# Performance work log

Hardware: AMD Instinct MI355X
Metric: run time of the kernel (lower is better)

Reference implementation:

```python
import jax, jax.numpy as jnp
import numpy as np

N_INST = 131072      # total patches across all bags
D_EMB = 512          # VGG16 pooling='max' output dim
ATT_UNITS = 128
CLS_UNITS = 512
NUM_BAGS = 256


def setup_inputs() -> dict:
    key = jax.random.key(0)
    ks = jax.random.split(key, 16)
    first_emb = jax.random.normal(ks[0], (N_INST, D_EMB), dtype=jnp.float32)
    first_lab = jnp.sort(jax.random.randint(ks[1], (N_INST,), 0, NUM_BAGS)).astype(jnp.int64)
    s = 0.02
    return {
        "first_emb": first_emb,
        "first_lab": first_lab,
        # first-level attention head: Dense(tanh) -> Dense(1, sigmoid)
        "W_a1": jax.random.normal(ks[2], (D_EMB, ATT_UNITS), dtype=jnp.float32) * s,
        "b_a1": jnp.zeros((ATT_UNITS,), dtype=jnp.float32),
        "w_o1": jax.random.normal(ks[3], (ATT_UNITS, 1), dtype=jnp.float32) * s,
        "b_o1": jnp.zeros((1,), dtype=jnp.float32),
        # second-level attention head
        "W_a2": jax.random.normal(ks[4], (D_EMB, ATT_UNITS), dtype=jnp.float32) * s,
        "b_a2": jnp.zeros((ATT_UNITS,), dtype=jnp.float32),
        "w_o2": jax.random.normal(ks[5], (ATT_UNITS, 1), dtype=jnp.float32) * s,
        "b_o2": jnp.zeros((1,), dtype=jnp.float32),
        # classifier: Dense(CLS_UNITS, linear) -> Dense(1, sigmoid)
        "W_c": jax.random.normal(ks[6], (D_EMB, CLS_UNITS), dtype=jnp.float32) * s,
        "b_c": jnp.zeros((CLS_UNITS,), dtype=jnp.float32),
        "w_out": jax.random.normal(ks[7], (CLS_UNITS, 1), dtype=jnp.float32) * s,
        "b_out": jnp.zeros((1,), dtype=jnp.float32),
    }


def reference(first_emb, first_lab, W_a1, b_a1, w_o1, b_o1,
              W_a2, b_a2, w_o2, b_o2, W_c, b_c, w_out, b_out):
    # --- first-level (instance) attention ---
    a1 = jnp.tanh(first_emb @ W_a1 + b_a1)                 # [N, A]
    att1 = jax.nn.sigmoid(a1 @ w_o1 + b_o1)                # [N, 1]
    # tf: transpose(softmax(transpose(att))) == softmax over the N axis (global)
    fst_att = jax.nn.softmax(att1, axis=0)                 # [N, 1]
    # --- per-bag attention-weighted sum (fused segment reduce) ---
    # replaces the python loop of gather_nd + matmul over contiguous bags
    second_emb = jax.ops.segment_sum(fst_att * first_emb, first_lab,
                                     num_segments=NUM_BAGS)  # [B, D]
    # --- second-level (bag) attention ---
    a2 = jnp.tanh(second_emb @ W_a2 + b_a2)                # [B, A]
    att2 = jax.nn.sigmoid(a2 @ w_o2 + b_o2)                # [B, 1]
    snd_att = jax.nn.softmax(att2.T, axis=-1)              # [1, B]
    outer_bag_emb = snd_att @ second_emb                   # [1, D]
    # --- classifier (dropout is identity at inference) ---
    h = outer_bag_emb @ W_c + b_c                          # [1, CLS]
    pred = jax.nn.sigmoid(h @ w_out + b_out)               # [1, 1]
    return pred
```

## Files before the change

kernel.cpp:

```cpp
#include <hip/hip_runtime.h>
#include <cstdint>
#include <cstddef>

#define N_INST 131072
#define D_EMB  512
#define ATT    128
#define NBAGS  256
#define TILE_I 32
#define LDA    520

typedef __attribute__((ext_vector_type(8))) short  bf16x8;
typedef __attribute__((ext_vector_type(4))) float  f32x4;
typedef __attribute__((ext_vector_type(4))) unsigned short u16x4;


__device__ inline unsigned short f2b(float f) {
    unsigned u = __builtin_bit_cast(unsigned, f);
    u += 0x7FFFu + ((u >> 16) & 1u);
    return (unsigned short)(u >> 16);
}

__device__ inline float fast_tanh(float x) {
    float e = __expf(2.f * x);
    return 1.f - 2.f / (e + 1.f);
}

__global__ __launch_bounds__(256) void k_prep_wt(
    const float* __restrict__ Wa1, unsigned short* __restrict__ Wt)
{
    const int n = blockIdx.x;
    for (int k = threadIdx.x; k < D_EMB; k += 256)
        Wt[(size_t)n * D_EMB + k] = f2b(Wa1[(size_t)k * ATT + n]);
}

__global__ __launch_bounds__(256, 4) void k_att1(
    const float* __restrict__ emb, const int* __restrict__ lab,
    const unsigned short* __restrict__ Wt, const float* __restrict__ ba1,
    const float* __restrict__ wo1, const float* __restrict__ bo1,
    float* __restrict__ rawr, int R, float* __restrict__ Z1)
{
    __shared__ unsigned short Ash[TILE_I * LDA];
    __shared__ float att4[4][TILE_I];
    __shared__ float sval[TILE_I];
    __shared__ int   labs[TILE_I];

    const int t  = threadIdx.x;
    const int w  = t >> 6;
    const int l  = t & 63;
    const int l4 = l & 15;
    const int h4 = l >> 4;
    const size_t i0 = (size_t)blockIdx.x * TILE_I;
    float* __restrict__ raw = rawr + (size_t)(blockIdx.x % R) * (NBAGS * D_EMB);

    if (t < TILE_I) labs[t] = lab[i0 + t];

    float ba1v[2], wo1v[2];
    #pragma unroll
    for (int nt = 0; nt < 2; ++nt) {
        int c = 16 * (2 * w + nt) + l4;
        ba1v[nt] = ba1[c];
        wo1v[nt] = wo1[c];
    }

    bf16x8 bfrag[2][16];
    #pragma unroll
    for (int nt = 0; nt < 2; ++nt) {
        const int n = 16 * (2 * w + nt) + l4;
        #pragma unroll
        for (int ks = 0; ks < 16; ++ks)
            bfrag[nt][ks] = *reinterpret_cast<const bf16x8*>(
                &Wt[(size_t)n * D_EMB + 32 * ks + 8 * h4]);
    }

    #pragma unroll
    for (int g = 0; g < 2; ++g) {
        float4 v[8];
        #pragma unroll
        for (int j = 0; j < 8; ++j) {
            int idx = (g * 8 + j) * 256 + t;
            int row = idx >> 7;
            int c4  = (idx & 127) * 4;
            v[j] = *reinterpret_cast<const float4*>(&emb[(i0 + row) * D_EMB + c4]);
        }
        #pragma unroll
        for (int j = 0; j < 8; ++j) {
            int idx = (g * 8 + j) * 256 + t;
            int row = idx >> 7;
            int c4  = (idx & 127) * 4;
            u16x4 b = { f2b(v[j].x), f2b(v[j].y), f2b(v[j].z), f2b(v[j].w) };
            *reinterpret_cast<u16x4*>(&Ash[row * LDA + c4]) = b;
        }
    }
    __syncthreads();

    f32x4 acc[2][2];
    #pragma unroll
    for (int rt = 0; rt < 2; ++rt) {
        acc[rt][0] = (f32x4){0.f, 0.f, 0.f, 0.f};
        acc[rt][1] = (f32x4){0.f, 0.f, 0.f, 0.f};
    }
    #pragma unroll
    for (int rt = 0; rt < 2; ++rt) {
        #pragma unroll
        for (int ks = 0; ks < 16; ++ks) {
            bf16x8 af = *reinterpret_cast<const bf16x8*>(
                &Ash[(16 * rt + l4) * LDA + 32 * ks + 8 * h4]);
            acc[rt][0] = __builtin_amdgcn_mfma_f32_16x16x32_bf16(
                af, bfrag[0][ks], acc[rt][0], 0, 0, 0);
            acc[rt][1] = __builtin_amdgcn_mfma_f32_16x16x32_bf16(
                af, bfrag[1][ks], acc[rt][1], 0, 0, 0);
        }
    }

    #pragma unroll
    for (int rt = 0; rt < 2; ++rt) {
        #pragma unroll
        for (int reg = 0; reg < 4; ++reg) {
            float p = fast_tanh(acc[rt][0][reg] + ba1v[0]) * wo1v[0]
                    + fast_tanh(acc[rt][1][reg] + ba1v[1]) * wo1v[1];
            p += __shfl_xor(p, 1);
            p += __shfl_xor(p, 2);
            p += __shfl_xor(p, 4);
            p += __shfl_xor(p, 8);
            if (l4 == 0) att4[w][16 * rt + 4 * h4 + reg] = p;
        }
    }
    __syncthreads();
    if (t < TILE_I) {
        float a  = att4[0][t] + att4[1][t] + att4[2][t] + att4[3][t] + bo1[0];
        float sg = 1.f / (1.f + __expf(-a));
        sval[t]  = __expf(sg);
    }
    __syncthreads();
    if (t < TILE_I) {
        float z = sval[t];
        z += __shfl_xor(z, 1);
        z += __shfl_xor(z, 2);
        z += __shfl_xor(z, 4);
        z += __shfl_xor(z, 8);
        z += __shfl_xor(z, 16);
        if (t == 0) atomicAdd(Z1, z);
    }

    int s0 = 0;
    while (s0 < TILE_I) {
        int bag = labs[s0];
        int s1 = s0 + 1;
        while (s1 < TILE_I && labs[s1] == bag) ++s1;
        float a0 = 0.f, a1 = 0.f;
        #pragma unroll 8
        for (int ii = s0; ii < s1; ++ii) {
            unsigned u = *reinterpret_cast<const unsigned*>(
                &Ash[(size_t)ii * LDA + 2 * t]);
            float lo = __builtin_bit_cast(float, u << 16);
            float hi = __builtin_bit_cast(float, u & 0xffff0000u);
            float s  = sval[ii];
            a0 = fmaf(s, lo, a0);
            a1 = fmaf(s, hi, a1);
        }
        atomicAdd(&raw[bag * D_EMB + 2 * t], a0);
        atomicAdd(&raw[bag * D_EMB + 2 * t + 1], a1);
        s0 = s1;
    }
}

__global__ __launch_bounds__(128) void k_att2(
    const float* __restrict__ Wa2, const float* __restrict__ ba2,
    const float* __restrict__ wo2, const float* __restrict__ bo2,
    float* __restrict__ rawr, int R, const float* __restrict__ Z1,
    float* __restrict__ e2, float* __restrict__ Z2)
{
    __shared__ float sec[D_EMB];
    __shared__ float hh[2];
    const int b = blockIdx.x;
    const int t = threadIdx.x;
    const float zinv = 1.f / Z1[0];
    for (int d = t; d < D_EMB; d += 128) {
        float s = 0.f;
        for (int r = 0; r < R; ++r)
            s += rawr[(size_t)r * (NBAGS * D_EMB) + b * D_EMB + d];
        float v = s * zinv;
        rawr[b * D_EMB + d] = v;
        sec[d] = v;
    }
    __syncthreads();
    float dot = 0.f;
    #pragma unroll 8
    for (int d = 0; d < D_EMB; ++d) dot = fmaf(sec[d], Wa2[d * ATT + t], dot);
    float h = fast_tanh(dot + ba2[t]) * wo2[t];
    #pragma unroll
    for (int m = 1; m < 64; m <<= 1) h += __shfl_xor(h, m);
    if ((t & 63) == 0) hh[t >> 6] = h;
    __syncthreads();
    if (t == 0) {
        float a  = hh[0] + hh[1] + bo2[0];
        float sg = 1.f / (1.f + __expf(-a));
        float e  = __expf(sg);
        e2[b] = e;
        atomicAdd(Z2, e);
    }
}

__global__ __launch_bounds__(256) void k_v(
    const float* __restrict__ Wc, const float* __restrict__ wout,
    float* __restrict__ v)
{
    const int t   = threadIdx.x;
    const int row = blockIdx.x * 8 + (t >> 5);
    const int l   = t & 31;
    float s = 0.f;
    #pragma unroll 4
    for (int c = l; c < 512; c += 32) s = fmaf(Wc[(size_t)row * 512 + c], wout[c], s);
    #pragma unroll
    for (int m = 1; m < 32; m <<= 1) s += __shfl_xor(s, m);
    if (l == 0) v[row] = s;
}

__global__ __launch_bounds__(256) void k_pool(
    const float* __restrict__ raw, const float* __restrict__ e2,
    float* __restrict__ outer)
{
    const int t  = threadIdx.x;
    const int b0 = blockIdx.x * 32;
    float o0 = 0.f, o1 = 0.f;
    for (int b = b0; b < b0 + 32; ++b) {
        float wgt = e2[b];
        float2 r = *reinterpret_cast<const float2*>(&raw[b * D_EMB + 2 * t]);
        o0 = fmaf(wgt, r.x, o0);
        o1 = fmaf(wgt, r.y, o1);
    }
    atomicAdd(&outer[2 * t], o0);
    atomicAdd(&outer[2 * t + 1], o1);
}

__global__ __launch_bounds__(256) void k_cls(
    const float* __restrict__ outer, const float* __restrict__ Z2,
    const float* __restrict__ v, const float* __restrict__ bc,
    const float* __restrict__ wout, const float* __restrict__ bout,
    float* __restrict__ out)
{
    __shared__ float pp[4];
    const int t = threadIdx.x;
    const float z2inv = 1.f / Z2[0];
    float p = (outer[2 * t] * v[2 * t] + outer[2 * t + 1] * v[2 * t + 1]) * z2inv
            + bc[2 * t] * wout[2 * t] + bc[2 * t + 1] * wout[2 * t + 1];
    #pragma unroll
    for (int m = 1; m < 64; m <<= 1) p += __shfl_xor(p, m);
    if ((t & 63) == 0) pp[t >> 6] = p;
    __syncthreads();
    if (t == 0) {
        float s = pp[0] + pp[1] + pp[2] + pp[3] + bout[0];
        out[0] = 1.f / (1.f + __expf(-s));
    }
}

extern "C" void kernel_launch(void* const* d_in, const int* in_sizes, int n_in,
                              void* d_out, int out_size, void* d_ws, size_t ws_size,
                              hipStream_t stream)
{
    const float* emb  = (const float*)d_in[0];
    const int*   lab  = (const int*)d_in[1];
    const float* Wa1  = (const float*)d_in[2];
    const float* ba1  = (const float*)d_in[3];
    const float* wo1  = (const float*)d_in[4];
    const float* bo1  = (const float*)d_in[5];
    const float* Wa2  = (const float*)d_in[6];
    const float* ba2  = (const float*)d_in[7];
    const float* wo2  = (const float*)d_in[8];
    const float* bo2  = (const float*)d_in[9];
    const float* Wc   = (const float*)d_in[10];
    const float* bc   = (const float*)d_in[11];
    const float* wout = (const float*)d_in[12];
    const float* bout = (const float*)d_in[13];

    float* ws    = (float*)d_ws;
    float* Z1    = ws + 0;
    float* Z2    = ws + 1;
    float* v     = ws + 16;
    float* e2    = ws + 1024;
    float* outer = ws + 1536;
    unsigned short* Wt = (unsigned short*)(ws + 4096);
    float* rawr  = ws + 36864;

    const size_t need8 = ((size_t)36864 + 8u * NBAGS * D_EMB) * sizeof(float);
    const int R = (ws_size >= need8) ? 8 : 1;

    hipMemsetAsync(d_ws, 0, ((size_t)36864 + (size_t)R * NBAGS * D_EMB) * sizeof(float), stream);

    hipLaunchKernelGGL(k_prep_wt, dim3(ATT),             dim3(256), 0, stream, Wa1, Wt);
    hipLaunchKernelGGL(k_v,       dim3(64),              dim3(256), 0, stream, Wc, wout, v);
    hipLaunchKernelGGL(k_att1,    dim3(N_INST / TILE_I), dim3(256), 0, stream,
                       emb, lab, Wt, ba1, wo1, bo1, rawr, R, Z1);
    hipLaunchKernelGGL(k_att2,    dim3(NBAGS),           dim3(128), 0, stream,
                       Wa2, ba2, wo2, bo2, rawr, R, Z1, e2, Z2);
    hipLaunchKernelGGL(k_pool,    dim3(8),               dim3(256), 0, stream,
                       rawr, e2, outer);
    hipLaunchKernelGGL(k_cls,     dim3(1),               dim3(256), 0, stream,
                       outer, Z2, v, bc, wout, bout, (float*)d_out);
}
```

Measured before the change: 166.3 us.

## Make att1 persistent with double-buffered LDS prefetch of embedding tiles

Turns k_att1 into a persistent kernel of 512 blocks, each looping over 8 tiles. The next tile's fp32 embeddings are loaded into registers while the current tile's MFMA, attention and segment reduction run, then converted to bf16 into a second LDS buffer. Z1 is accumulated per block and written with one atomic at the end. Costs are B fragments reloaded from global/L2 on every tile instead of kept in registers, doubled LDS use with occupancy lowered to 2 blocks per SIMD setting, and 16 float4 registers held live for the prefetch.

```diff
diff --git a/kernel.cpp b/kernel.cpp
--- a/kernel.cpp
+++ b/kernel.cpp
@@ -8,6 +8,9 @@
 #define NBAGS  256
 #define TILE_I 32
 #define LDA    520
+#define NBLK   512
+#define NTILES (N_INST / TILE_I)
+#define TPB    (NTILES / NBLK)
 
 typedef __attribute__((ext_vector_type(8))) short  bf16x8;
 typedef __attribute__((ext_vector_type(4))) float  f32x4;
@@ -33,135 +36,155 @@
         Wt[(size_t)n * D_EMB + k] = f2b(Wa1[(size_t)k * ATT + n]);
 }
 
-__global__ __launch_bounds__(256, 4) void k_att1(
+__global__ __launch_bounds__(256, 2) void k_att1(
     const float* __restrict__ emb, const int* __restrict__ lab,
     const unsigned short* __restrict__ Wt, const float* __restrict__ ba1,
     const float* __restrict__ wo1, const float* __restrict__ bo1,
     float* __restrict__ rawr, int R, float* __restrict__ Z1)
 {
-    __shared__ unsigned short Ash[TILE_I * LDA];
+    __shared__ unsigned short Ash[2][TILE_I * LDA];
     __shared__ float att4[4][TILE_I];
     __shared__ float sval[TILE_I];
-    __shared__ int   labs[TILE_I];
+    __shared__ int   labs[2][TILE_I];
 
     const int t  = threadIdx.x;
     const int w  = t >> 6;
     const int l  = t & 63;
     const int l4 = l & 15;
     const int h4 = l >> 4;
-    const size_t i0 = (size_t)blockIdx.x * TILE_I;
+    const int n0 = 16 * (2 * w) + l4;
+    const int n1 = 16 * (2 * w + 1) + l4;
     float* __restrict__ raw = rawr + (size_t)(blockIdx.x % R) * (NBAGS * D_EMB);
 
-    if (t < TILE_I) labs[t] = lab[i0 + t];
-
-    float ba1v[2], wo1v[2];
-    #pragma unroll
-    for (int nt = 0; nt < 2; ++nt) {
-        int c = 16 * (2 * w + nt) + l4;
-        ba1v[nt] = ba1[c];
-        wo1v[nt] = wo1[c];
-    }
-
-    bf16x8 bfrag[2][16];
-    #pragma unroll
-    for (int nt = 0; nt < 2; ++nt) {
-        const int n = 16 * (2 * w + nt) + l4;
+    const float ba1v0 = ba1[n0], ba1v1 = ba1[n1];
+    const float wo1v0 = wo1[n0], wo1v1 = wo1[n1];
+    float z1acc = 0.f;
+
+    {
+        const size_t i0 = (size_t)blockIdx.x * TILE_I;
+        float4 v[16];
         #pragma unroll
-        for (int ks = 0; ks < 16; ++ks)
-            bfrag[nt][ks] = *reinterpret_cast<const bf16x8*>(
-                &Wt[(size_t)n * D_EMB + 32 * ks + 8 * h4]);
-    }
-
-    #pragma unroll
-    for (int g = 0; g < 2; ++g) {
-        float4 v[8];
-        #pragma unroll
-        for (int j = 0; j < 8; ++j) {
-            int idx = (g * 8 + j) * 256 + t;
+        for (int j = 0; j < 16; ++j) {
+            int idx = j * 256 + t;
             int row = idx >> 7;
             int c4  = (idx & 127) * 4;
             v[j] = *reinterpret_cast<const float4*>(&emb[(i0 + row) * D_EMB + c4]);
         }
+        if (t < TILE_I) labs[0][t] = lab[i0 + t];
         #pragma unroll
-        for (int j = 0; j < 8; ++j) {
-            int idx = (g * 8 + j) * 256 + t;
+        for (int j = 0; j < 16; ++j) {
+            int idx = j * 256 + t;
             int row = idx >> 7;
             int c4  = (idx & 127) * 4;
             u16x4 b = { f2b(v[j].x), f2b(v[j].y), f2b(v[j].z), f2b(v[j].w) };
-            *reinterpret_cast<u16x4*>(&Ash[row * LDA + c4]) = b;
+            *reinterpret_cast<u16x4*>(&Ash[0][row * LDA + c4]) = b;
         }
     }
     __syncthreads();
 
-    f32x4 acc[2][2];
-    #pragma unroll
-    for (int rt = 0; rt < 2; ++rt) {
-        acc[rt][0] = (f32x4){0.f, 0.f, 0.f, 0.f};
-        acc[rt][1] = (f32x4){0.f, 0.f, 0.f, 0.f};
-    }
-    #pragma unroll
-    for (int rt = 0; rt < 2; ++rt) {
+    int p = 0;
+    for (int it = 0; it < TPB; ++it) {
+        const bool hasNext = (it + 1 < TPB);
+        const size_t i0n = ((size_t)blockIdx.x + (size_t)(it + 1) * NBLK) * TILE_I;
+
+        float4 v[16];
+        int nlab = 0;
+        if (hasNext) {
+            #pragma unroll
+            for (int j = 0; j < 16; ++j) {
+                int idx = j * 256 + t;
+                int row = idx >> 7;
+                int c4  = (idx & 127) * 4;
+                v[j] = *reinterpret_cast<const float4*>(
+                    &emb[(i0n + row) * D_EMB + c4]);
+            }
+            if (t < TILE_I) nlab = lab[i0n + t];
+        }
+
+        f32x4 acc00 = {0.f,0.f,0.f,0.f}, acc01 = {0.f,0.f,0.f,0.f};
+        f32x4 acc10 = {0.f,0.f,0.f,0.f}, acc11 = {0.f,0.f,0.f,0.f};
         #pragma unroll
         for (int ks = 0; ks < 16; ++ks) {
-            bf16x8 af = *reinterpret_cast<const bf16x8*>(
-                &Ash[(16 * rt + l4) * LDA + 32 * ks + 8 * h4]);
-            acc[rt][0] = __builtin_amdgcn_mfma_f32_16x16x32_bf16(
-                af, bfrag[0][ks], acc[rt][0], 0, 0, 0);
-            acc[rt][1] = __builtin_amdgcn_mfma_f32_16x16x32_bf16(
-                af, bfrag[1][ks], acc[rt][1], 0, 0, 0);
-        }
-    }
-
-    #pragma unroll
-    for (int rt = 0; rt < 2; ++rt) {
+            bf16x8 b0 = *reinterpret_cast<const bf16x8*>(
+                &Wt[(size_t)n0 * D_EMB + 32 * ks + 8 * h4]);
+            bf16x8 b1 = *reinterpret_cast<const bf16x8*>(
+                &Wt[(size_t)n1 * D_EMB + 32 * ks + 8 * h4]);
+            bf16x8 a0 = *reinterpret_cast<const bf16x8*>(
+                &Ash[p][(l4) * LDA + 32 * ks + 8 * h4]);
+            bf16x8 a1 = *reinterpret_cast<const bf16x8*>(
+                &Ash[p][(16 + l4) * LDA + 32 * ks + 8 * h4]);
+            acc00 = __builtin_amdgcn_mfma_f32_16x16x32_bf16(a0, b0, acc00, 0, 0, 0);
+            acc01 = __builtin_amdgcn_mfma_f32_16x16x32_bf16(a0, b1, acc01, 0, 0, 0);
+            acc10 = __builtin_amdgcn_mfma_f32_16x16x32_bf16(a1, b0, acc10, 0, 0, 0);
+            acc11 = __builtin_amdgcn_mfma_f32_16x16x32_bf16(a1, b1, acc11, 0, 0, 0);
+        }
+
         #pragma unroll
-        for (int reg = 0; reg < 4; ++reg) {
-            float p = fast_tanh(acc[rt][0][reg] + ba1v[0]) * wo1v[0]
-                    + fast_tanh(acc[rt][1][reg] + ba1v[1]) * wo1v[1];
-            p += __shfl_xor(p, 1);
-            p += __shfl_xor(p, 2);
-            p += __shfl_xor(p, 4);
-            p += __shfl_xor(p, 8);
-            if (l4 == 0) att4[w][16 * rt + 4 * h4 + reg] = p;
-        }
-    }
-    __syncthreads();
-    if (t < TILE_I) {
-        float a  = att4[0][t] + att4[1][t] + att4[2][t] + att4[3][t] + bo1[0];
-        float sg = 1.f / (1.f + __expf(-a));
-        sval[t]  = __expf(sg);
-    }
-    __syncthreads();
-    if (t < TILE_I) {
-        float z = sval[t];
-        z += __shfl_xor(z, 1);
-        z += __shfl_xor(z, 2);
-        z += __shfl_xor(z, 4);
-        z += __shfl_xor(z, 8);
-        z += __shfl_xor(z, 16);
-        if (t == 0) atomicAdd(Z1, z);
-    }
-
-    int s0 = 0;
-    while (s0 < TILE_I) {
-        int bag = labs[s0];
-        int s1 = s0 + 1;
-        while (s1 < TILE_I && labs[s1] == bag) ++s1;
-        float a0 = 0.f, a1 = 0.f;
-        #pragma unroll 8
-        for (int ii = s0; ii < s1; ++ii) {
-            unsigned u = *reinterpret_cast<const unsigned*>(
-                &Ash[(size_t)ii * LDA + 2 * t]);
-            float lo = __builtin_bit_cast(float, u << 16);
-            float hi = __builtin_bit_cast(float, u & 0xffff0000u);
-            float s  = sval[ii];
-            a0 = fmaf(s, lo, a0);
-            a1 = fmaf(s, hi, a1);
-        }
-        atomicAdd(&raw[bag * D_EMB + 2 * t], a0);
-        atomicAdd(&raw[bag * D_EMB + 2 * t + 1], a1);
-        s0 = s1;
-    }
+        for (int rt = 0; rt < 2; ++rt) {
+            #pragma unroll
+            for (int reg = 0; reg < 4; ++reg) {
+                float pp = fast_tanh((rt ? acc10[reg] : acc00[reg]) + ba1v0) * wo1v0
+                         + fast_tanh((rt ? acc11[reg] : acc01[reg]) + ba1v1) * wo1v1;
+                pp += __shfl_xor(pp, 1);
+                pp += __shfl_xor(pp, 2);
+                pp += __shfl_xor(pp, 4);
+                pp += __shfl_xor(pp, 8);
+                if (l4 == 0) att4[w][16 * rt + 4 * h4 + reg] = pp;
+            }
+        }
+        __syncthreads();
+        if (t < TILE_I) {
+            float a  = att4[0][t] + att4[1][t] + att4[2][t] + att4[3][t] + bo1[0];
+            float sg = 1.f / (1.f + __expf(-a));
+            sval[t]  = __expf(sg);
+        }
+        __syncthreads();
+        if (t < TILE_I) {
+            float z = sval[t];
+            z += __shfl_xor(z, 1);
+            z += __shfl_xor(z, 2);
+            z += __shfl_xor(z, 4);
+            z += __shfl_xor(z, 8);
+            z += __shfl_xor(z, 16);
+            if (t == 0) z1acc += z;
+        }
+
+        int s0 = 0;
+        while (s0 < TILE_I) {
+            int bag = labs[p][s0];
+            int s1 = s0 + 1;
+            while (s1 < TILE_I && labs[p][s1] == bag) ++s1;
+            float a0 = 0.f, a1 = 0.f;
+            for (int ii = s0; ii < s1; ++ii) {
+                unsigned u = *reinterpret_cast<const unsigned*>(
+                    &Ash[p][(size_t)ii * LDA + 2 * t]);
+                float lo = __builtin_bit_cast(float, u << 16);
+                float hi = __builtin_bit_cast(float, u & 0xffff0000u);
+                float s  = sval[ii];
+                a0 = fmaf(s, lo, a0);
+                a1 = fmaf(s, hi, a1);
+            }
+            atomicAdd(&raw[bag * D_EMB + 2 * t], a0);
+            atomicAdd(&raw[bag * D_EMB + 2 * t + 1], a1);
+            s0 = s1;
+        }
+        __syncthreads();
+
+        if (hasNext) {
+            #pragma unroll
+            for (int j = 0; j < 16; ++j) {
+                int idx = j * 256 + t;
+                int row = idx >> 7;
+                int c4  = (idx & 127) * 4;
+                u16x4 b = { f2b(v[j].x), f2b(v[j].y), f2b(v[j].z), f2b(v[j].w) };
+                *reinterpret_cast<u16x4*>(&Ash[p ^ 1][row * LDA + c4]) = b;
+            }
+            if (t < TILE_I) labs[p ^ 1][t] = nlab;
+        }
+        __syncthreads();
+        p ^= 1;
+    }
+    if (t == 0) atomicAdd(Z1, z1acc);
 }
 
 __global__ __launch_bounds__(128) void k_att2(
@@ -287,14 +310,14 @@
 
     hipMemsetAsync(d_ws, 0, ((size_t)36864 + (size_t)R * NBAGS * D_EMB) * sizeof(float), stream);
 
-    hipLaunchKernelGGL(k_prep_wt, dim3(ATT),             dim3(256), 0, stream, Wa1, Wt);
-    hipLaunchKernelGGL(k_v,       dim3(64),              dim3(256), 0, stream, Wc, wout, v);
-    hipLaunchKernelGGL(k_att1,    dim3(N_INST / TILE_I), dim3(256), 0, stream,
+    hipLaunchKernelGGL(k_prep_wt, dim3(ATT),   dim3(256), 0, stream, Wa1, Wt);
+    hipLaunchKernelGGL(k_v,       dim3(64),    dim3(256), 0, stream, Wc, wout, v);
+    hipLaunchKernelGGL(k_att1,    dim3(NBLK),  dim3(256), 0, stream,
                        emb, lab, Wt, ba1, wo1, bo1, rawr, R, Z1);
-    hipLaunchKernelGGL(k_att2,    dim3(NBAGS),           dim3(128), 0, stream,
+    hipLaunchKernelGGL(k_att2,    dim3(NBAGS), dim3(128), 0, stream,
                        Wa2, ba2, wo2, bo2, rawr, R, Z1, e2, Z2);
-    hipLaunchKernelGGL(k_pool,    dim3(8),               dim3(256), 0, stream,
+    hipLaunchKernelGGL(k_pool,    dim3(8),     dim3(256), 0, stream,
                        rawr, e2, outer);
-    hipLaunchKernelGGL(k_cls,     dim3(1),               dim3(256), 0, stream,
+    hipLaunchKernelGGL(k_cls,     dim3(1),     dim3(256), 0, stream,
                        outer, Z2, v, bc, wout, bout, (float*)d_out);
 }
```

Result: faster. 136.0 us (-18.3%).
